# Kernel optimization log

Measured on AMD Instinct MI355X. Metric: run time of the kernel, lower is better.

The kernel has to match this reference:

```python
import jax, jax.numpy as jnp
import numpy as np

N_NODES = 100000
N_EDGES = 1600000
N_GRAPHS = 256
EPS = 1e-5  # GraphNorm / BatchNorm eps


def _seg_sum(x, seg, n):
    return jax.ops.segment_sum(x, seg, num_segments=n)


def setup_inputs() -> dict:
    key = jax.random.key(0)
    ks = jax.random.split(key, 24)
    f32 = jnp.float32

    def nrm(k, shape, s=0.05):
        return jax.random.normal(k, shape, f32) * s

    inp = {}
    inp["x"] = jax.random.normal(ks[0], (N_NODES, 64), f32)
    inp["edge_attr"] = jax.random.normal(ks[1], (N_EDGES, 8), f32)
    # edge_mlp: Linear(8,16) -> ReLU -> Linear(16,1); final bias +2 keeps degrees positive
    inp["em_w1"] = nrm(ks[2], (16, 8), 0.1); inp["em_b1"] = jnp.zeros((16,), f32)
    inp["em_w2"] = nrm(ks[3], (1, 16), 0.1); inp["em_b2"] = jnp.full((1,), 2.0, f32)
    # GCNConv weights stored (in, out); PyG GCNConv lin has no bias, separate bias after aggregation
    inp["conv_w0"] = nrm(ks[4], (64, 128)); inp["conv_b0"] = jnp.zeros((128,), f32)
    inp["conv_w1"] = nrm(ks[5], (128, 128)); inp["conv_b1"] = jnp.zeros((128,), f32)
    inp["conv_w2"] = nrm(ks[6], (128, 128)); inp["conv_b2"] = jnp.zeros((128,), f32)
    # GraphNorm params: weight=1, bias=0, mean_scale=1 (PyG init)
    for i in range(3):
        inp[f"gn_w{i}"] = jnp.ones((128,), f32)
        inp[f"gn_b{i}"] = jnp.zeros((128,), f32)
        inp[f"gn_ms{i}"] = jnp.ones((128,), f32)
    # MLP head (weights stored (in,out)); BatchNorm1d eval: running_mean=0, running_var=1
    inp["lin_w0"] = nrm(ks[7], (128, 256)); inp["lin_b0"] = jnp.zeros((256,), f32)
    inp["bn_g0"] = jnp.ones((256,), f32); inp["bn_b0"] = jnp.zeros((256,), f32)
    inp["lin_w1"] = nrm(ks[8], (256, 128)); inp["lin_b1"] = jnp.zeros((128,), f32)
    inp["bn_g1"] = jnp.ones((128,), f32); inp["bn_b1"] = jnp.zeros((128,), f32)
    inp["out_w"] = nrm(ks[9], (128, 1)); inp["out_b"] = jnp.zeros((1,), f32)
    inp["edge_index"] = jax.random.randint(ks[10], (2, N_EDGES), 0, N_NODES)
    inp["batch"] = jnp.sort(jax.random.randint(ks[11], (N_NODES,), 0, N_GRAPHS))
    return inp


def _gcn_conv(h, W, b, src, tgt, ew):
    # PyG GCNConv with edge_weight: add self-loops (weight 1), symmetric normalization
    hw = h @ W  # [N, out]
    deg = _seg_sum(ew, tgt, N_NODES) + 1.0  # in-degree incl. self-loop
    dinv = jnp.where(deg > 0, jax.lax.rsqrt(deg), 0.0)
    norm_e = dinv[src] * ew * dinv[tgt]  # [E]
    agg = _seg_sum(norm_e[:, None] * hw[src], tgt, N_NODES)
    agg = agg + (dinv * dinv)[:, None] * hw  # self-loop contribution
    return agg + b


def _graph_norm(h, batch, w, b, ms, cnt):
    mean = _seg_sum(h, batch, N_GRAPHS) / cnt[:, None]  # [G, C]
    sub = h - ms * mean[batch]
    var = _seg_sum(sub * sub, batch, N_GRAPHS) / cnt[:, None]
    return w * sub / jnp.sqrt(var + EPS)[batch] + b


def reference(x, edge_attr, em_w1, em_b1, em_w2, em_b2,
              conv_w0, conv_b0, conv_w1, conv_b1, conv_w2, conv_b2,
              gn_w0, gn_b0, gn_ms0, gn_w1, gn_b1, gn_ms1, gn_w2, gn_b2, gn_ms2,
              lin_w0, lin_b0, bn_g0, bn_b0, lin_w1, lin_b1, bn_g1, bn_b1,
              out_w, out_b, edge_index, batch):
    src, tgt = edge_index[0], edge_index[1]
    ew = (jax.nn.relu(edge_attr @ em_w1.T + em_b1) @ em_w2.T + em_b2).reshape(-1)  # [E]
    cnt = jnp.maximum(_seg_sum(jnp.ones((N_NODES,), x.dtype), batch, N_GRAPHS), 1.0)

    h = x
    layers = [(conv_w0, conv_b0, gn_w0, gn_b0, gn_ms0),
              (conv_w1, conv_b1, gn_w1, gn_b1, gn_ms1),
              (conv_w2, conv_b2, gn_w2, gn_b2, gn_ms2)]
    for W, b, gw, gb, gms in layers:
        h = _gcn_conv(h, W, b, src, tgt, ew)
        h = _graph_norm(h, batch, gw, gb, gms, cnt)
        h = jax.nn.relu(h)  # dropout is identity in eval mode

    pooled = _seg_sum(h, batch, N_GRAPHS) / cnt[:, None]  # global_mean_pool [G, 128]

    inv = 1.0 / jnp.sqrt(1.0 + EPS)  # BatchNorm1d eval: mean=0, var=1
    h = jax.nn.relu((pooled @ lin_w0 + lin_b0) * inv * bn_g0 + bn_b0)
    h = jax.nn.relu((h @ lin_w1 + lin_b1) * inv * bn_g1 + bn_b1)
    out = h @ out_w + out_b  # [G, 1]
    return (out, h)
```

## Files before the change

kernel.cpp:

```cpp
#include <hip/hip_runtime.h>

#define N_NODES 100000
#define N_EDGES 1600000
#define N_GRAPHS 256
#define EPS 1e-5f

#define NBUCK 1024
#define NUSED 782
#define NBLK 128
#define EPB (N_EDGES / NBLK)

#define EB 6250
#define WB 128
#define W0B 32
#define PREP_BLOCKS (EB + WB + W0B + 2)

typedef __attribute__((ext_vector_type(8))) short bfrag8;
typedef __attribute__((ext_vector_type(4))) float facc4;

__device__ __forceinline__ void fma4(float4& a, float s, const float4& w) {
  a.x += s * w.x; a.y += s * w.y; a.z += s * w.z; a.w += s * w.w;
}

__device__ __forceinline__ unsigned short f2bf(float f) {
  union { float f; unsigned u; } x;
  x.f = f;
  unsigned r = x.u + 0x7FFF + ((x.u >> 16) & 1);
  return (unsigned short)(r >> 16);
}
__device__ __forceinline__ unsigned packbf(float a, float b) {
  return (unsigned)f2bf(a) | ((unsigned)f2bf(b) << 16);
}
__device__ __forceinline__ float4 bf4(unsigned lo, unsigned hi) {
  union { unsigned u; float f; } a, b, c, d;
  a.u = lo << 16;
  b.u = lo & 0xFFFF0000u;
  c.u = hi << 16;
  d.u = hi & 0xFFFF0000u;
  return make_float4(a.f, b.f, c.f, d.f);
}
__device__ __forceinline__ float bfat(const unsigned* tb, int idx) {
  unsigned u = tb[idx >> 1];
  union { unsigned u; float f; } v;
  v.u = (idx & 1) ? (u & 0xFFFF0000u) : (u << 16);
  return v.f;
}

__global__ __launch_bounds__(256) void k_prep(
    const float* __restrict__ ea, const float* __restrict__ w1,
    const float* __restrict__ b1, const float* __restrict__ w2,
    const float* __restrict__ b2, float* __restrict__ ew,
    const float* __restrict__ cw1, const float* __restrict__ cw2,
    unsigned short* __restrict__ wt1, unsigned short* __restrict__ wt2,
    const float* __restrict__ cw0, unsigned short* __restrict__ wt0,
    const int* __restrict__ batch, int* __restrict__ start) {
  __shared__ float W1[128], B1[16], W2[16];
  const int b = blockIdx.x;
  const int t = threadIdx.x;
  if (b < EB) {
    if (t < 128) W1[t] = w1[t];
    if (t < 16) { B1[t] = b1[t]; W2[t] = w2[t]; }
    __syncthreads();
    int e = b * 256 + t;
    if (e >= N_EDGES) return;
    const float4* ap = (const float4*)(ea + (size_t)e * 8);
    float4 a0 = ap[0], a1 = ap[1];
    float a[8] = {a0.x, a0.y, a0.z, a0.w, a1.x, a1.y, a1.z, a1.w};
    float out = b2[0];
#pragma unroll
    for (int i = 0; i < 16; ++i) {
      float h = B1[i];
#pragma unroll
      for (int j = 0; j < 8; ++j) h += a[j] * W1[i * 8 + j];
      out += fmaxf(h, 0.f) * W2[i];
    }
    ew[e] = out;
  } else if (b < EB + WB) {
    int lb = b - EB;
    int half = lb >> 6;
    int id = (lb & 63) * 256 + t;
    const float* w = half ? cw2 : cw1;
    unsigned short* o = half ? wt2 : wt1;
    int n = id >> 7, k = id & 127;
    o[n * 128 + k] = f2bf(w[k * 128 + n]);
  } else if (b < EB + WB + W0B) {
    int id = (b - EB - WB) * 256 + t;
    if (id >= 8192) return;
    int n = id >> 6, k = id & 63;
    wt0[n * 64 + k] = f2bf(cw0[k * 128 + n]);
  } else {
    int g = (b - EB - WB - W0B) * 256 + t;
    if (g > N_GRAPHS) return;
    int lo = 0, hi = N_NODES;
    while (lo < hi) {
      int mid = (lo + hi) >> 1;
      if (batch[mid] < g) lo = mid + 1; else hi = mid;
    }
    start[g] = lo;
  }
}

__global__ __launch_bounds__(256) void k_hist(const int* __restrict__ tgt,
                                              int* __restrict__ hists) {
  __shared__ int h[NBUCK];
  const int blk = blockIdx.x, t = threadIdx.x;
  for (int i = t; i < NBUCK; i += 256) h[i] = 0;
  __syncthreads();
  const int s = blk * EPB, e = s + EPB;
  for (int j = s + t; j < e; j += 256) atomicAdd(&h[tgt[j] >> 7], 1);
  __syncthreads();
  for (int i = t; i < NBUCK; i += 256) hists[blk * NBUCK + i] = h[i];
}

__global__ __launch_bounds__(1024) void k_bscan(const int* __restrict__ hists,
                                                int* __restrict__ bbase,
                                                int* __restrict__ cursor) {
  __shared__ int s[NBUCK];
  const int b = threadIdx.x;
  int tot = 0;
  for (int k = 0; k < NBLK; ++k) tot += hists[k * NBUCK + b];
  s[b] = tot;
  __syncthreads();
  for (int off = 1; off < NBUCK; off <<= 1) {
    int u = (b >= off) ? s[b - off] : 0;
    __syncthreads();
    s[b] += u;
    __syncthreads();
  }
  int base = s[b] - tot;
  bbase[b] = base;
  if (b == NBUCK - 1) bbase[NBUCK] = N_EDGES;
  int c = base;
  for (int k = 0; k < NBLK; ++k) {
    cursor[k * NBUCK + b] = c;
    c += hists[k * NBUCK + b];
  }
}

__global__ __launch_bounds__(256) void k_scatter(
    const int* __restrict__ src, const int* __restrict__ tgt,
    const float* __restrict__ ew, const int* __restrict__ cursor,
    uint2* __restrict__ mb) {
  __shared__ int cur[NBUCK];
  const int blk = blockIdx.x, t = threadIdx.x;
  for (int i = t; i < NBUCK; i += 256) cur[i] = cursor[blk * NBUCK + i];
  __syncthreads();
  const int s = blk * EPB, e = s + EPB;
  for (int j = s + t; j < e; j += 256) {
    int d = tgt[j];
    int bin = d >> 7;
    int pos = atomicAdd(&cur[bin], 1);
    union { float f; unsigned u; } w;
    w.f = ew[j];
    mb[pos] = make_uint2(w.u, (unsigned)src[j] | ((unsigned)(d & 127) << 25));
  }
}

__global__ __launch_bounds__(256) void k_csr(const uint2* __restrict__ mb,
                                             const int* __restrict__ bbase,
                                             uint2* __restrict__ meta,
                                             int* __restrict__ rowstart) {
  __shared__ int hist[128];
  __shared__ int cur[128];
  const int b = blockIdx.x;
  const int t = threadIdx.x;
  const int s = bbase[b], e = bbase[b + 1];
  if (t < 128) hist[t] = 0;
  __syncthreads();
  for (int j = s + t; j < e; j += 256)
    atomicAdd(&hist[mb[j].y >> 25], 1);
  __syncthreads();
  int own = (t < 128) ? hist[t] : 0;
  for (int off = 1; off < 128; off <<= 1) {
    int u = (t >= off && t < 128) ? hist[t - off] : 0;
    __syncthreads();
    if (t < 128) hist[t] += u;
    __syncthreads();
  }
  if (t < 128) {
    int excl = hist[t] - own;
    int node = b * 128 + t;
    if (node <= N_NODES) rowstart[node] = s + excl;
    cur[t] = s + excl;
  }
  __syncthreads();
  for (int j = s + t; j < e; j += 256) {
    uint2 m = mb[j];
    int bin = m.y >> 25;
    int pos = atomicAdd(&cur[bin], 1);
    meta[pos] = make_uint2(m.x, m.y & 0x1FFFFFFu);
  }
}

__global__ __launch_bounds__(256) void k_degcvt(
    const uint2* __restrict__ meta, const int* __restrict__ rowstart,
    const float* __restrict__ x, float* __restrict__ dinv,
    unsigned* __restrict__ xb) {
  const int n = blockIdx.x * 4 + (threadIdx.x >> 6);
  if (n >= N_NODES) return;
  const int lane = threadIdx.x & 63;
  const int rs = rowstart[n], re = rowstart[n + 1];
  float s = 0.f;
  for (int j = rs + lane; j < re; j += 64) {
    union { unsigned u; float f; } w;
    w.u = meta[j].x;
    s += w.f;
  }
#pragma unroll
  for (int m = 1; m < 64; m <<= 1) s += __shfl_xor(s, m);
  float d = 1.f + s;
  float dv = d > 0.f ? rsqrtf(d) : 0.f;
  if (lane == 0) dinv[n] = dv;
  if (lane < 32) {
    float2 v = ((const float2*)x)[(size_t)n * 32 + lane];
    xb[((unsigned)n << 5) + lane] = packbf(dv * v.x, dv * v.y);
  }
}

__global__ __launch_bounds__(256) void k_gather64b(
    const unsigned* __restrict__ xb, const uint2* __restrict__ meta,
    const int* __restrict__ rowstart, const float* __restrict__ dinv,
    unsigned* __restrict__ aggxb) {
  const int t = threadIdx.x;
  const int n = blockIdx.x * 4 + (t >> 6);
  if (n >= N_NODES) return;
  const unsigned lane = t & 63;
  const unsigned q = lane >> 3;
  const unsigned cl = lane & 7;
  const int rs = rowstart[n], re = rowstart[n + 1];
  const uint4* x4 = (const uint4*)xb;
  float4 lo0 = make_float4(0.f, 0.f, 0.f, 0.f), hi0 = lo0;
  float4 lo1 = lo0, hi1 = lo0;
  int j = rs;
  for (; j + 16 <= re; j += 16) {
    uint2 m0 = meta[j + q], m1 = meta[j + 8 + q];
    union { unsigned u; float f; } w0, w1;
    w0.u = m0.x; w1.u = m1.x;
    uint4 v0 = x4[(m0.y << 3) + cl];
    uint4 v1 = x4[(m1.y << 3) + cl];
    fma4(lo0, w0.f, bf4(v0.x, v0.y));
    fma4(hi0, w0.f, bf4(v0.z, v0.w));
    fma4(lo1, w1.f, bf4(v1.x, v1.y));
    fma4(hi1, w1.f, bf4(v1.z, v1.w));
  }
  for (; j + 8 <= re; j += 8) {
    uint2 m0 = meta[j + q];
    union { unsigned u; float f; } w0;
    w0.u = m0.x;
    uint4 v0 = x4[(m0.y << 3) + cl];
    fma4(lo0, w0.f, bf4(v0.x, v0.y));
    fma4(hi0, w0.f, bf4(v0.z, v0.w));
  }
  if (j + (int)q < re) {
    uint2 m0 = meta[j + q];
    union { unsigned u; float f; } w0;
    w0.u = m0.x;
    uint4 v0 = x4[(m0.y << 3) + cl];
    fma4(lo1, w0.f, bf4(v0.x, v0.y));
    fma4(hi1, w0.f, bf4(v0.z, v0.w));
  }
  lo0.x += lo1.x; lo0.y += lo1.y; lo0.z += lo1.z; lo0.w += lo1.w;
  hi0.x += hi1.x; hi0.y += hi1.y; hi0.z += hi1.z; hi0.w += hi1.w;
#pragma unroll
  for (int m = 8; m <= 32; m <<= 1) {
    lo0.x += __shfl_xor(lo0.x, m);
    lo0.y += __shfl_xor(lo0.y, m);
    lo0.z += __shfl_xor(lo0.z, m);
    lo0.w += __shfl_xor(lo0.w, m);
    hi0.x += __shfl_xor(hi0.x, m);
    hi0.y += __shfl_xor(hi0.y, m);
    hi0.z += __shfl_xor(hi0.z, m);
    hi0.w += __shfl_xor(hi0.w, m);
  }
  if (q == 0) {
    float dv = dinv[n];
    uint4 sv = x4[((unsigned)n << 3) + cl];
    float4 slo = bf4(sv.x, sv.y), shi = bf4(sv.z, sv.w);
    uint4 o;
    o.x = packbf(dv * (lo0.x + slo.x), dv * (lo0.y + slo.y));
    o.y = packbf(dv * (lo0.z + slo.z), dv * (lo0.w + slo.w));
    o.z = packbf(dv * (hi0.x + shi.x), dv * (hi0.y + shi.y));
    o.w = packbf(dv * (hi0.z + shi.z), dv * (hi0.w + shi.w));
    ((uint4*)aggxb)[((unsigned)n << 3) + cl] = o;
  }
}

__global__ __launch_bounds__(256) void k_hw_mfma0(
    const unsigned short* __restrict__ aggxb,
    const unsigned short* __restrict__ wt0, const float* __restrict__ bias,
    unsigned short* __restrict__ h1b) {
  __shared__ unsigned short Asb[64][72];
  __shared__ unsigned short Wsb[128][72];
  const int t = threadIdx.x;
  const int base = blockIdx.x * 64;

  for (int i = t; i < 1024; i += 256) {
    int nr = i >> 3, k8 = (i & 7) * 8;
    *(uint4*)&Wsb[nr][k8] = *(const uint4*)&wt0[nr * 64 + k8];
  }
  {
    const int ln = t >> 2;
    const int kp = (t & 3) * 16;
    const int n = base + ln;
    if (n < N_NODES) {
      *(uint4*)&Asb[ln][kp] = *(const uint4*)&aggxb[(size_t)n * 64 + kp];
      *(uint4*)&Asb[ln][kp + 8] = *(const uint4*)&aggxb[(size_t)n * 64 + kp + 8];
    } else {
      uint4 z = make_uint4(0, 0, 0, 0);
      *(uint4*)&Asb[ln][kp] = z;
      *(uint4*)&Asb[ln][kp + 8] = z;
    }
  }
  __syncthreads();

  const int wv = t >> 6;
  const int lr = t & 15;
  const int lk = (t >> 4) & 3;
  const int m0 = wv * 16;

  bfrag8 af[2];
#pragma unroll
  for (int kc = 0; kc < 2; ++kc)
    af[kc] = *(const bfrag8*)&Asb[m0 + lr][kc * 32 + lk * 8];

#pragma unroll
  for (int nt = 0; nt < 8; ++nt) {
    facc4 c = {0.f, 0.f, 0.f, 0.f};
#pragma unroll
    for (int kc = 0; kc < 2; ++kc) {
      bfrag8 bf = *(const bfrag8*)&Wsb[nt * 16 + lr][kc * 32 + lk * 8];
      c = __builtin_amdgcn_mfma_f32_16x16x32_bf16(af[kc], bf, c, 0, 0, 0);
    }
    int col = nt * 16 + lr;
    float bv = bias[col];
#pragma unroll
    for (int r = 0; r < 4; ++r) {
      int n = base + m0 + lk * 4 + r;
      if (n < N_NODES) h1b[(size_t)n * 128 + col] = f2bf(c[r] + bv);
    }
  }
}

__global__ __launch_bounds__(256) void k_hw_mfma(
    const unsigned* __restrict__ hb, const unsigned short* __restrict__ wt,
    const int* __restrict__ batch, const float* __restrict__ An,
    const float* __restrict__ Bn, const float* __restrict__ dinv,
    unsigned short* __restrict__ hwb) {
  __shared__ unsigned short Asb[64][136];
  __shared__ unsigned short Wsb[128][136];
  const int t = threadIdx.x;
  const int base = blockIdx.x * 64;

  for (int i = t; i < 2048; i += 256) {
    int nr = i >> 4, k8 = (i & 15) * 8;
    *(uint4*)&Wsb[nr][k8] = *(const uint4*)&wt[nr * 128 + k8];
  }
  {
    const int ln = t >> 2;
    const int cg = (t & 3) * 32;
    const int n = base + ln;
    if (n < N_NODES) {
      const int g = batch[n];
      const uint4* hp = (const uint4*)(hb + (size_t)n * 64);
      const float* Ap = An + (size_t)g * 128;
      const float* Bp = Bn + (size_t)g * 128;
#pragma unroll
      for (int qq = 0; qq < 4; ++qq) {
        int c = cg + qq * 8;
        uint4 v = hp[(t & 3) * 4 + qq];
        float4 lo = bf4(v.x, v.y);
        float4 hi = bf4(v.z, v.w);
        float4 Alo = *(const float4*)&Ap[c], Blo = *(const float4*)&Bp[c];
        float4 Ahi = *(const float4*)&Ap[c + 4], Bhi = *(const float4*)&Bp[c + 4];
        uint4 o;
        o.x = packbf(fmaxf(Alo.x * lo.x + Blo.x, 0.f),
                     fmaxf(Alo.y * lo.y + Blo.y, 0.f));
        o.y = packbf(fmaxf(Alo.z * lo.z + Blo.z, 0.f),
                     fmaxf(Alo.w * lo.w + Blo.w, 0.f));
        o.z = packbf(fmaxf(Ahi.x * hi.x + Bhi.x, 0.f),
                     fmaxf(Ahi.y * hi.y + Bhi.y, 0.f));
        o.w = packbf(fmaxf(Ahi.z * hi.z + Bhi.z, 0.f),
                     fmaxf(Ahi.w * hi.w + Bhi.w, 0.f));
        *(uint4*)&Asb[ln][c] = o;
      }
    } else {
      uint4 z = make_uint4(0, 0, 0, 0);
#pragma unroll
      for (int qq = 0; qq < 4; ++qq) *(uint4*)&Asb[ln][cg + qq * 8] = z;
    }
  }
  __syncthreads();

  const int wv = t >> 6;
  const int lr = t & 15;
  const int lk = (t >> 4) & 3;
  const int m0 = wv * 16;

  bfrag8 af[4];
#pragma unroll
  for (int kc = 0; kc < 4; ++kc)
    af[kc] = *(const bfrag8*)&Asb[m0 + lr][kc * 32 + lk * 8];

  float dv[4];
#pragma unroll
  for (int r = 0; r < 4; ++r) {
    int n = base + m0 + lk * 4 + r;
    dv[r] = (n < N_NODES) ? dinv[n] : 0.f;
  }

#pragma unroll
  for (int nt = 0; nt < 8; ++nt) {
    facc4 c = {0.f, 0.f, 0.f, 0.f};
#pragma unroll
    for (int kc = 0; kc < 4; ++kc) {
      bfrag8 bf = *(const bfrag8*)&Wsb[nt * 16 + lr][kc * 32 + lk * 8];
      c = __builtin_amdgcn_mfma_f32_16x16x32_bf16(af[kc], bf, c, 0, 0, 0);
    }
    int col = nt * 16 + lr;
#pragma unroll
    for (int r = 0; r < 4; ++r) {
      int n = base + m0 + lk * 4 + r;
      if (n < N_NODES) hwb[(size_t)n * 128 + col] = f2bf(dv[r] * c[r]);
    }
  }
}

__global__ __launch_bounds__(256) void k_gatherb(
    const unsigned* __restrict__ hwb, const uint2* __restrict__ meta,
    const int* __restrict__ rowstart, const float* __restrict__ dinv,
    const float* __restrict__ bias, unsigned* __restrict__ aggb) {
  const int t = threadIdx.x;
  const int n = blockIdx.x * 4 + (t >> 6);
  if (n >= N_NODES) return;
  const unsigned lane = t & 63;
  const unsigned q = lane >> 4;
  const unsigned cl = lane & 15;
  const int rs = rowstart[n], re = rowstart[n + 1];
  const uint4* hb4 = (const uint4*)hwb;
  float4 lo0 = make_float4(0.f, 0.f, 0.f, 0.f), hi0 = lo0;
  float4 lo1 = lo0, hi1 = lo0;
  int j = rs;
  for (; j + 8 <= re; j += 8) {
    uint2 m0 = meta[j + q], m1 = meta[j + 4 + q];
    union { unsigned u; float f; } w0, w1;
    w0.u = m0.x; w1.u = m1.x;
    uint4 v0 = hb4[(m0.y << 4) + cl];
    uint4 v1 = hb4[(m1.y << 4) + cl];
    fma4(lo0, w0.f, bf4(v0.x, v0.y));
    fma4(hi0, w0.f, bf4(v0.z, v0.w));
    fma4(lo1, w1.f, bf4(v1.x, v1.y));
    fma4(hi1, w1.f, bf4(v1.z, v1.w));
  }
  for (; j + 4 <= re; j += 4) {
    uint2 m0 = meta[j + q];
    union { unsigned u; float f; } w0;
    w0.u = m0.x;
    uint4 v0 = hb4[(m0.y << 4) + cl];
    fma4(lo0, w0.f, bf4(v0.x, v0.y));
    fma4(hi0, w0.f, bf4(v0.z, v0.w));
  }
  if (j + (int)q < re) {
    uint2 m0 = meta[j + q];
    union { unsigned u; float f; } w0;
    w0.u = m0.x;
    uint4 v0 = hb4[(m0.y << 4) + cl];
    fma4(lo1, w0.f, bf4(v0.x, v0.y));
    fma4(hi1, w0.f, bf4(v0.z, v0.w));
  }
  lo0.x += lo1.x; lo0.y += lo1.y; lo0.z += lo1.z; lo0.w += lo1.w;
  hi0.x += hi1.x; hi0.y += hi1.y; hi0.z += hi1.z; hi0.w += hi1.w;
#pragma unroll
  for (int m = 16; m <= 32; m <<= 1) {
    lo0.x += __shfl_xor(lo0.x, m);
    lo0.y += __shfl_xor(lo0.y, m);
    lo0.z += __shfl_xor(lo0.z, m);
    lo0.w += __shfl_xor(lo0.w, m);
    hi0.x += __shfl_xor(hi0.x, m);
    hi0.y += __shfl_xor(hi0.y, m);
    hi0.z += __shfl_xor(hi0.z, m);
    hi0.w += __shfl_xor(hi0.w, m);
  }
  if (q == 0) {
    float dv = dinv[n];
    uint4 sv = hb4[((unsigned)n << 4) + cl];
    float4 slo = bf4(sv.x, sv.y), shi = bf4(sv.z, sv.w);
    float4 blo = *(const float4*)&bias[cl * 8];
    float4 bhi = *(const float4*)&bias[cl * 8 + 4];
    uint4 o;
    o.x = packbf(dv * (lo0.x + slo.x) + blo.x, dv * (lo0.y + slo.y) + blo.y);
    o.y = packbf(dv * (lo0.z + slo.z) + blo.z, dv * (lo0.w + slo.w) + blo.w);
    o.z = packbf(dv * (hi0.x + shi.x) + bhi.x, dv * (hi0.y + shi.y) + bhi.y);
    o.w = packbf(dv * (hi0.z + shi.z) + bhi.z, dv * (hi0.w + shi.w) + bhi.w);
    ((uint4*)aggb)[((unsigned)n << 4) + cl] = o;
  }
}

__global__ __launch_bounds__(512) void k_gstats(
    const unsigned* __restrict__ hb, const int* __restrict__ start,
    const float* __restrict__ gw, const float* __restrict__ gb,
    const float* __restrict__ gms, float* __restrict__ An,
    float* __restrict__ Bn) {
  int g = blockIdx.x;
  int s = start[g], e = start[g + 1];
  int t = threadIdx.x, p = t >> 7, c = t & 127;
  float sum = 0.f, sq = 0.f;
  for (int n = s + p; n < e; n += 4) {
    float v = bfat(hb + (size_t)n * 64, c);
    sum += v;
    sq += v * v;
  }
  __shared__ float S[4][128], Q[4][128];
  S[p][c] = sum;
  Q[p][c] = sq;
  __syncthreads();
  if (t < 128) {
    float cnt = (float)max(e - s, 1);
    float mean = (S[0][t] + S[1][t] + S[2][t] + S[3][t]) / cnt;
    float e2 = (Q[0][t] + Q[1][t] + Q[2][t] + Q[3][t]) / cnt;
    float ms = gms[t];
    float var = fmaxf(e2 - ms * (2.f - ms) * mean * mean, 0.f);
    float scale = gw[t] / sqrtf(var + EPS);
    An[(size_t)g * 128 + t] = scale;
    Bn[(size_t)g * 128 + t] = gb[t] - scale * ms * mean;
  }
}

__global__ __launch_bounds__(512) void k_pool(
    const unsigned* __restrict__ hb, const int* __restrict__ start,
    const float* __restrict__ An, const float* __restrict__ Bn,
    float* __restrict__ pooled) {
  int g = blockIdx.x;
  int s = start[g], e = start[g + 1];
  int t = threadIdx.x, p = t >> 7, c = t & 127;
  float A = An[(size_t)g * 128 + c], B = Bn[(size_t)g * 128 + c];
  float sum = 0.f;
  for (int n = s + p; n < e; n += 4)
    sum += fmaxf(A * bfat(hb + (size_t)n * 64, c) + B, 0.f);
  __shared__ float S[4][128];
  S[p][c] = sum;
  __syncthreads();
  if (t < 128) {
    float cnt = (float)max(e - s, 1);
    pooled[g * 128 + t] = (S[0][t] + S[1][t] + S[2][t] + S[3][t]) / cnt;
  }
}

__global__ __launch_bounds__(256) void k_head(
    const float* __restrict__ pooled, const float* __restrict__ w0,
    const float* __restrict__ b0, const float* __restrict__ g0,
    const float* __restrict__ bb0, const float* __restrict__ w1,
    const float* __restrict__ b1, const float* __restrict__ g1,
    const float* __restrict__ bb1, const float* __restrict__ ow,
    const float* __restrict__ ob, float* __restrict__ out) {
  __shared__ float p[128], h1[256], h2[128];
  int g = blockIdx.x, t = threadIdx.x;
  const float inv = 1.0f / sqrtf(1.0f + EPS);
  if (t < 128) p[t] = pooled[g * 128 + t];
  __syncthreads();
  {
    float acc = b0[t];
#pragma unroll 8
    for (int k = 0; k < 128; ++k) acc += p[k] * w0[k * 256 + t];
    h1[t] = fmaxf(acc * inv * g0[t] + bb0[t], 0.f);
  }
  __syncthreads();
  if (t < 128) {
    float acc = b1[t];
#pragma unroll 8
    for (int k = 0; k < 256; ++k) acc += h1[k] * w1[k * 128 + t];
    float v = fmaxf(acc * inv * g1[t] + bb1[t], 0.f);
    h2[t] = v;
    out[N_GRAPHS + g * 128 + t] = v;
  }
  __syncthreads();
  if (t < 64) {
    float v = h2[t] * ow[t] + h2[t + 64] * ow[t + 64];
#pragma unroll
    for (int off = 32; off; off >>= 1) v += __shfl_down(v, off);
    if (t == 0) out[g] = v + ob[0];
  }
}

extern "C" void kernel_launch(void* const* d_in, const int* in_sizes, int n_in,
                              void* d_out, int out_size, void* d_ws,
                              size_t ws_size, hipStream_t stream) {
  const float* x = (const float*)d_in[0];
  const float* edge_attr = (const float*)d_in[1];
  const float* em_w1 = (const float*)d_in[2];
  const float* em_b1 = (const float*)d_in[3];
  const float* em_w2 = (const float*)d_in[4];
  const float* em_b2 = (const float*)d_in[5];
  const float* conv_w[3] = {(const float*)d_in[6], (const float*)d_in[8],
                            (const float*)d_in[10]};
  const float* conv_b[3] = {(const float*)d_in[7], (const float*)d_in[9],
                            (const float*)d_in[11]};
  const float* gn_w[3] = {(const float*)d_in[12], (const float*)d_in[15],
                          (const float*)d_in[18]};
  const float* gn_b[3] = {(const float*)d_in[13], (const float*)d_in[16],
                          (const float*)d_in[19]};
  const float* gn_ms[3] = {(const float*)d_in[14], (const float*)d_in[17],
                           (const float*)d_in[20]};
  const float* lin_w0 = (const float*)d_in[21];
  const float* lin_b0 = (const float*)d_in[22];
  const float* bn_g0 = (const float*)d_in[23];
  const float* bn_b0 = (const float*)d_in[24];
  const float* lin_w1 = (const float*)d_in[25];
  const float* lin_b1 = (const float*)d_in[26];
  const float* bn_g1 = (const float*)d_in[27];
  const float* bn_b1 = (const float*)d_in[28];
  const float* out_w = (const float*)d_in[29];
  const float* out_b = (const float*)d_in[30];
  const int* edge_index = (const int*)d_in[31];
  const int* batch = (const int*)d_in[32];
  const int* src = edge_index;
  const int* tgt = edge_index + N_EDGES;

  char* w = (char*)d_ws;
  size_t off = 0;
  auto carve = [&](size_t bytes) {
    void* p = w + off;
    off = (off + bytes + 511) & ~(size_t)511;
    return p;
  };
  float* ew = (float*)carve((size_t)N_EDGES * 4);
  float* dinv = (float*)carve((size_t)N_NODES * 4);
  int* rowstart = (int*)carve((size_t)(N_NODES + 1) * 4);
  int* hists = (int*)carve((size_t)NBLK * NBUCK * 4);
  int* cursor = (int*)carve((size_t)NBLK * NBUCK * 4);
  int* bbase = (int*)carve((size_t)(NBUCK + 1) * 4);
  uint2* mb = (uint2*)carve((size_t)N_EDGES * 8);
  uint2* meta = (uint2*)carve((size_t)N_EDGES * 8);
  int* start = (int*)carve((N_GRAPHS + 1) * 4);
  float* AB = (float*)carve((size_t)6 * N_GRAPHS * 128 * 4);
  unsigned* xb = (unsigned*)carve((size_t)N_NODES * 64 * 2);
  unsigned* aggxb = (unsigned*)carve((size_t)N_NODES * 64 * 2);
  unsigned* h1b = (unsigned*)carve((size_t)N_NODES * 128 * 2);
  unsigned* hwb = (unsigned*)carve((size_t)N_NODES * 128 * 2);
  unsigned* agg1b = (unsigned*)carve((size_t)N_NODES * 128 * 2);
  unsigned* agg2b = (unsigned*)carve((size_t)N_NODES * 128 * 2);
  unsigned short* wt0 = (unsigned short*)carve((size_t)128 * 64 * 2);
  unsigned short* wt1 = (unsigned short*)carve((size_t)128 * 128 * 2);
  unsigned short* wt2 = (unsigned short*)carve((size_t)128 * 128 * 2);
  float* pooled = (float*)carve((size_t)N_GRAPHS * 128 * 4);

  float* A0 = AB, *B0 = AB + N_GRAPHS * 128;
  float* A1 = AB + 2 * N_GRAPHS * 128, *B1 = AB + 3 * N_GRAPHS * 128;
  float* A2 = AB + 4 * N_GRAPHS * 128, *B2 = AB + 5 * N_GRAPHS * 128;

  k_prep<<<PREP_BLOCKS, 256, 0, stream>>>(
      edge_attr, em_w1, em_b1, em_w2, em_b2, ew, conv_w[1], conv_w[2], wt1,
      wt2, conv_w[0], wt0, batch, start);
  k_hist<<<NBLK, 256, 0, stream>>>(tgt, hists);
  k_bscan<<<1, 1024, 0, stream>>>(hists, bbase, cursor);
  k_scatter<<<NBLK, 256, 0, stream>>>(src, tgt, ew, cursor, mb);
  k_csr<<<NUSED, 256, 0, stream>>>(mb, bbase, meta, rowstart);

  const int ggrid = (N_NODES + 3) / 4;
  const int hwgrid = (N_NODES + 63) / 64;

  k_degcvt<<<ggrid, 256, 0, stream>>>(meta, rowstart, x, dinv, xb);

  k_gather64b<<<ggrid, 256, 0, stream>>>(xb, meta, rowstart, dinv, aggxb);
  k_hw_mfma0<<<hwgrid, 256, 0, stream>>>((unsigned short*)aggxb, wt0,
                                         conv_b[0], (unsigned short*)h1b);
  k_gstats<<<N_GRAPHS, 512, 0, stream>>>(h1b, start, gn_w[0], gn_b[0],
                                         gn_ms[0], A0, B0);
  k_hw_mfma<<<hwgrid, 256, 0, stream>>>(h1b, wt1, batch, A0, B0, dinv,
                                        (unsigned short*)hwb);
  k_gatherb<<<ggrid, 256, 0, stream>>>(hwb, meta, rowstart, dinv, conv_b[1],
                                       agg1b);
  k_gstats<<<N_GRAPHS, 512, 0, stream>>>(agg1b, start, gn_w[1], gn_b[1],
                                         gn_ms[1], A1, B1);
  k_hw_mfma<<<hwgrid, 256, 0, stream>>>(agg1b, wt2, batch, A1, B1, dinv,
                                        (unsigned short*)hwb);
  k_gatherb<<<ggrid, 256, 0, stream>>>(hwb, meta, rowstart, dinv, conv_b[2],
                                       agg2b);
  k_gstats<<<N_GRAPHS, 512, 0, stream>>>(agg2b, start, gn_w[2], gn_b[2],
                                         gn_ms[2], A2, B2);

  k_pool<<<N_GRAPHS, 512, 0, stream>>>(agg2b, start, A2, B2, pooled);
  k_head<<<N_GRAPHS, 256, 0, stream>>>(pooled, lin_w0, lin_b0, bn_g0, bn_b0,
                                       lin_w1, lin_b1, bn_g1, bn_b1, out_w,
                                       out_b, (float*)d_out);
}
```

Baseline: 523.2 us.

## Fuse edge MLP into scatter, use global bucket cursors, fold degree into CSR

Moves the edge-weight MLP into the scatter kernel so the ew array is never written or read back. The per-block histogram and cursor tables are replaced by one global bucket count built with atomics and global atomic cursors in the scatter. The weighted degree is accumulated inside the CSR build with shared-memory float atomics, and the old per-node warp degree pass becomes a flat x-to-bf16 conversion kernel. This drops the separate histogram kernel and the degree pass, at the cost of heavily contended global atomics on 1024 cursors and a nondeterministic edge order inside each bucket.

```diff
diff --git a/kernel.cpp b/kernel.cpp
--- a/kernel.cpp
+++ b/kernel.cpp
@@ -7,13 +7,12 @@
 
 #define NBUCK 1024
 #define NUSED 782
-#define NBLK 128
-#define EPB (N_EDGES / NBLK)
-
-#define EB 6250
+
 #define WB 128
 #define W0B 32
-#define PREP_BLOCKS (EB + WB + W0B + 2)
+#define SB 2
+#define HB 512
+#define PREP_BLOCKS (WB + W0B + SB + HB)
 
 typedef __attribute__((ext_vector_type(8))) short bfrag8;
 typedef __attribute__((ext_vector_type(4))) float facc4;
@@ -47,49 +46,28 @@
 }
 
 __global__ __launch_bounds__(256) void k_prep(
-    const float* __restrict__ ea, const float* __restrict__ w1,
-    const float* __restrict__ b1, const float* __restrict__ w2,
-    const float* __restrict__ b2, float* __restrict__ ew,
     const float* __restrict__ cw1, const float* __restrict__ cw2,
     unsigned short* __restrict__ wt1, unsigned short* __restrict__ wt2,
     const float* __restrict__ cw0, unsigned short* __restrict__ wt0,
-    const int* __restrict__ batch, int* __restrict__ start) {
-  __shared__ float W1[128], B1[16], W2[16];
+    const int* __restrict__ batch, int* __restrict__ start,
+    const int* __restrict__ tgt, int* __restrict__ bcnt) {
+  __shared__ int h[NBUCK];
   const int b = blockIdx.x;
   const int t = threadIdx.x;
-  if (b < EB) {
-    if (t < 128) W1[t] = w1[t];
-    if (t < 16) { B1[t] = b1[t]; W2[t] = w2[t]; }
-    __syncthreads();
-    int e = b * 256 + t;
-    if (e >= N_EDGES) return;
-    const float4* ap = (const float4*)(ea + (size_t)e * 8);
-    float4 a0 = ap[0], a1 = ap[1];
-    float a[8] = {a0.x, a0.y, a0.z, a0.w, a1.x, a1.y, a1.z, a1.w};
-    float out = b2[0];
-#pragma unroll
-    for (int i = 0; i < 16; ++i) {
-      float h = B1[i];
-#pragma unroll
-      for (int j = 0; j < 8; ++j) h += a[j] * W1[i * 8 + j];
-      out += fmaxf(h, 0.f) * W2[i];
-    }
-    ew[e] = out;
-  } else if (b < EB + WB) {
-    int lb = b - EB;
-    int half = lb >> 6;
-    int id = (lb & 63) * 256 + t;
+  if (b < WB) {
+    int half = b >> 6;
+    int id = (b & 63) * 256 + t;
     const float* w = half ? cw2 : cw1;
     unsigned short* o = half ? wt2 : wt1;
     int n = id >> 7, k = id & 127;
     o[n * 128 + k] = f2bf(w[k * 128 + n]);
-  } else if (b < EB + WB + W0B) {
-    int id = (b - EB - WB) * 256 + t;
+  } else if (b < WB + W0B) {
+    int id = (b - WB) * 256 + t;
     if (id >= 8192) return;
     int n = id >> 6, k = id & 63;
     wt0[n * 64 + k] = f2bf(cw0[k * 128 + n]);
-  } else {
-    int g = (b - EB - WB - W0B) * 256 + t;
+  } else if (b < WB + W0B + SB) {
+    int g = (b - WB - W0B) * 256 + t;
     if (g > N_GRAPHS) return;
     int lo = 0, hi = N_NODES;
     while (lo < hi) {
@@ -97,29 +75,27 @@
       if (batch[mid] < g) lo = mid + 1; else hi = mid;
     }
     start[g] = lo;
-  }
-}
-
-__global__ __launch_bounds__(256) void k_hist(const int* __restrict__ tgt,
-                                              int* __restrict__ hists) {
-  __shared__ int h[NBUCK];
-  const int blk = blockIdx.x, t = threadIdx.x;
-  for (int i = t; i < NBUCK; i += 256) h[i] = 0;
-  __syncthreads();
-  const int s = blk * EPB, e = s + EPB;
-  for (int j = s + t; j < e; j += 256) atomicAdd(&h[tgt[j] >> 7], 1);
-  __syncthreads();
-  for (int i = t; i < NBUCK; i += 256) hists[blk * NBUCK + i] = h[i];
-}
-
-__global__ __launch_bounds__(1024) void k_bscan(const int* __restrict__ hists,
+  } else {
+    const int hb = b - WB - W0B - SB;
+    for (int i = t; i < NBUCK; i += 256) h[i] = 0;
+    __syncthreads();
+    for (int j = hb * 256 + t; j < N_EDGES; j += HB * 256)
+      atomicAdd(&h[tgt[j] >> 7], 1);
+    __syncthreads();
+    for (int i = t; i < NBUCK; i += 256) {
+      int v = h[i];
+      if (v) atomicAdd(&bcnt[i], v);
+    }
+  }
+}
+
+__global__ __launch_bounds__(1024) void k_bscan(const int* __restrict__ bcnt,
                                                 int* __restrict__ bbase,
-                                                int* __restrict__ cursor) {
+                                                int* __restrict__ gcur) {
   __shared__ int s[NBUCK];
   const int b = threadIdx.x;
-  int tot = 0;
-  for (int k = 0; k < NBLK; ++k) tot += hists[k * NBUCK + b];
-  s[b] = tot;
+  int v = bcnt[b];
+  s[b] = v;
   __syncthreads();
   for (int off = 1; off < NBUCK; off <<= 1) {
     int u = (b >= off) ? s[b - off] : 0;
@@ -127,48 +103,64 @@
     s[b] += u;
     __syncthreads();
   }
-  int base = s[b] - tot;
+  int base = s[b] - v;
   bbase[b] = base;
+  gcur[b] = base;
   if (b == NBUCK - 1) bbase[NBUCK] = N_EDGES;
-  int c = base;
-  for (int k = 0; k < NBLK; ++k) {
-    cursor[k * NBUCK + b] = c;
-    c += hists[k * NBUCK + b];
-  }
 }
 
 __global__ __launch_bounds__(256) void k_scatter(
-    const int* __restrict__ src, const int* __restrict__ tgt,
-    const float* __restrict__ ew, const int* __restrict__ cursor,
+    const float* __restrict__ ea, const float* __restrict__ w1,
+    const float* __restrict__ b1, const float* __restrict__ w2,
+    const float* __restrict__ b2, const int* __restrict__ src,
+    const int* __restrict__ tgt, int* __restrict__ gcur,
     uint2* __restrict__ mb) {
-  __shared__ int cur[NBUCK];
-  const int blk = blockIdx.x, t = threadIdx.x;
-  for (int i = t; i < NBUCK; i += 256) cur[i] = cursor[blk * NBUCK + i];
-  __syncthreads();
-  const int s = blk * EPB, e = s + EPB;
-  for (int j = s + t; j < e; j += 256) {
-    int d = tgt[j];
-    int bin = d >> 7;
-    int pos = atomicAdd(&cur[bin], 1);
-    union { float f; unsigned u; } w;
-    w.f = ew[j];
-    mb[pos] = make_uint2(w.u, (unsigned)src[j] | ((unsigned)(d & 127) << 25));
-  }
+  __shared__ float W1[128], B1[16], W2[16];
+  const int t = threadIdx.x;
+  if (t < 128) W1[t] = w1[t];
+  if (t < 16) { B1[t] = b1[t]; W2[t] = w2[t]; }
+  __syncthreads();
+  int e = blockIdx.x * 256 + t;
+  if (e >= N_EDGES) return;
+  const float4* ap = (const float4*)(ea + (size_t)e * 8);
+  float4 a0 = ap[0], a1 = ap[1];
+  float a[8] = {a0.x, a0.y, a0.z, a0.w, a1.x, a1.y, a1.z, a1.w};
+  float out = b2[0];
+#pragma unroll
+  for (int i = 0; i < 16; ++i) {
+    float h = B1[i];
+#pragma unroll
+    for (int j = 0; j < 8; ++j) h += a[j] * W1[i * 8 + j];
+    out += fmaxf(h, 0.f) * W2[i];
+  }
+  int d = tgt[e];
+  int pos = atomicAdd(&gcur[d >> 7], 1);
+  union { float f; unsigned u; } w;
+  w.f = out;
+  mb[pos] = make_uint2(w.u, (unsigned)src[e] | ((unsigned)(d & 127) << 25));
 }
 
 __global__ __launch_bounds__(256) void k_csr(const uint2* __restrict__ mb,
                                              const int* __restrict__ bbase,
                                              uint2* __restrict__ meta,
-                                             int* __restrict__ rowstart) {
+                                             int* __restrict__ rowstart,
+                                             float* __restrict__ dinv) {
   __shared__ int hist[128];
+  __shared__ float degf[128];
   __shared__ int cur[128];
   const int b = blockIdx.x;
   const int t = threadIdx.x;
   const int s = bbase[b], e = bbase[b + 1];
-  if (t < 128) hist[t] = 0;
-  __syncthreads();
-  for (int j = s + t; j < e; j += 256)
-    atomicAdd(&hist[mb[j].y >> 25], 1);
+  if (t < 128) { hist[t] = 0; degf[t] = 0.f; }
+  __syncthreads();
+  for (int j = s + t; j < e; j += 256) {
+    uint2 m = mb[j];
+    int bin = m.y >> 25;
+    atomicAdd(&hist[bin], 1);
+    union { unsigned u; float f; } w;
+    w.u = m.x;
+    atomicAdd(&degf[bin], w.f);
+  }
   __syncthreads();
   int own = (t < 128) ? hist[t] : 0;
   for (int off = 1; off < 128; off <<= 1) {
@@ -181,6 +173,10 @@
     int excl = hist[t] - own;
     int node = b * 128 + t;
     if (node <= N_NODES) rowstart[node] = s + excl;
+    if (node < N_NODES) {
+      float d = 1.f + degf[t];
+      dinv[node] = d > 0.f ? rsqrtf(d) : 0.f;
+    }
     cur[t] = s + excl;
   }
   __syncthreads();
@@ -192,29 +188,21 @@
   }
 }
 
-__global__ __launch_bounds__(256) void k_degcvt(
-    const uint2* __restrict__ meta, const int* __restrict__ rowstart,
-    const float* __restrict__ x, float* __restrict__ dinv,
-    unsigned* __restrict__ xb) {
-  const int n = blockIdx.x * 4 + (threadIdx.x >> 6);
-  if (n >= N_NODES) return;
-  const int lane = threadIdx.x & 63;
-  const int rs = rowstart[n], re = rowstart[n + 1];
-  float s = 0.f;
-  for (int j = rs + lane; j < re; j += 64) {
-    union { unsigned u; float f; } w;
-    w.u = meta[j].x;
-    s += w.f;
-  }
-#pragma unroll
-  for (int m = 1; m < 64; m <<= 1) s += __shfl_xor(s, m);
-  float d = 1.f + s;
-  float dv = d > 0.f ? rsqrtf(d) : 0.f;
-  if (lane == 0) dinv[n] = dv;
-  if (lane < 32) {
-    float2 v = ((const float2*)x)[(size_t)n * 32 + lane];
-    xb[((unsigned)n << 5) + lane] = packbf(dv * v.x, dv * v.y);
-  }
+__global__ __launch_bounds__(256) void k_cvt(const float* __restrict__ x,
+                                             const float* __restrict__ dinv,
+                                             unsigned* __restrict__ xb) {
+  int i = blockIdx.x * 256 + threadIdx.x;
+  if (i >= N_NODES * 8) return;
+  int n = i >> 3;
+  float dv = dinv[n];
+  const float4* p = (const float4*)(x + (size_t)i * 8);
+  float4 a = p[0], b = p[1];
+  uint4 o;
+  o.x = packbf(dv * a.x, dv * a.y);
+  o.y = packbf(dv * a.z, dv * a.w);
+  o.z = packbf(dv * b.x, dv * b.y);
+  o.w = packbf(dv * b.z, dv * b.w);
+  ((uint4*)xb)[i] = o;
 }
 
 __global__ __launch_bounds__(256) void k_gather64b(
@@ -622,12 +610,11 @@
     off = (off + bytes + 511) & ~(size_t)511;
     return p;
   };
-  float* ew = (float*)carve((size_t)N_EDGES * 4);
   float* dinv = (float*)carve((size_t)N_NODES * 4);
   int* rowstart = (int*)carve((size_t)(N_NODES + 1) * 4);
-  int* hists = (int*)carve((size_t)NBLK * NBUCK * 4);
-  int* cursor = (int*)carve((size_t)NBLK * NBUCK * 4);
+  int* bcnt = (int*)carve((size_t)NBUCK * 4);
   int* bbase = (int*)carve((size_t)(NBUCK + 1) * 4);
+  int* gcur = (int*)carve((size_t)NBUCK * 4);
   uint2* mb = (uint2*)carve((size_t)N_EDGES * 8);
   uint2* meta = (uint2*)carve((size_t)N_EDGES * 8);
   int* start = (int*)carve((N_GRAPHS + 1) * 4);
@@ -647,18 +634,19 @@
   float* A1 = AB + 2 * N_GRAPHS * 128, *B1 = AB + 3 * N_GRAPHS * 128;
   float* A2 = AB + 4 * N_GRAPHS * 128, *B2 = AB + 5 * N_GRAPHS * 128;
 
-  k_prep<<<PREP_BLOCKS, 256, 0, stream>>>(
-      edge_attr, em_w1, em_b1, em_w2, em_b2, ew, conv_w[1], conv_w[2], wt1,
-      wt2, conv_w[0], wt0, batch, start);
-  k_hist<<<NBLK, 256, 0, stream>>>(tgt, hists);
-  k_bscan<<<1, 1024, 0, stream>>>(hists, bbase, cursor);
-  k_scatter<<<NBLK, 256, 0, stream>>>(src, tgt, ew, cursor, mb);
-  k_csr<<<NUSED, 256, 0, stream>>>(mb, bbase, meta, rowstart);
+  hipMemsetAsync(bcnt, 0, (size_t)NBUCK * 4, stream);
+
+  k_prep<<<PREP_BLOCKS, 256, 0, stream>>>(conv_w[1], conv_w[2], wt1, wt2,
+                                          conv_w[0], wt0, batch, start, tgt,
+                                          bcnt);
+  k_bscan<<<1, 1024, 0, stream>>>(bcnt, bbase, gcur);
+  k_scatter<<<(N_EDGES + 255) / 256, 256, 0, stream>>>(
+      edge_attr, em_w1, em_b1, em_w2, em_b2, src, tgt, gcur, mb);
+  k_csr<<<NUSED, 256, 0, stream>>>(mb, bbase, meta, rowstart, dinv);
+  k_cvt<<<(N_NODES * 8 + 255) / 256, 256, 0, stream>>>(x, dinv, xb);
 
   const int ggrid = (N_NODES + 3) / 4;
   const int hwgrid = (N_NODES + 63) / 64;
-
-  k_degcvt<<<ggrid, 256, 0, stream>>>(meta, rowstart, x, dinv, xb);
 
   k_gather64b<<<ggrid, 256, 0, stream>>>(xb, meta, rowstart, dinv, aggxb);
   k_hw_mfma0<<<hwgrid, 256, 0, stream>>>((unsigned short*)aggxb, wt0,
```

Result: slower. 812.4 us (+55.3%).
